# Kernel optimization log

Measured on AMD Instinct MI355X. Metric: run time of the kernel, lower is better.

The kernel has to match this reference:

```python
import jax, jax.numpy as jnp
import numpy as np

B, C, N = 4, 3, 8192

def setup_inputs() -> dict:
    key = jax.random.key(0)
    k1, k2, k3 = jax.random.split(key, 3)
    return {
        "registration_pred": jax.random.normal(k1, (B, C, N), dtype=jnp.float32),
        "registration_gt": jax.random.normal(k2, (B, C, N), dtype=jnp.float32),
        "coords": jax.random.normal(k3, (B, C, N), dtype=jnp.float32),
    }

def reference(registration_pred, registration_gt, coords):
    # point clouds: [B, N, 3]
    pc1 = jnp.transpose(coords + registration_gt, (0, 2, 1))   # gt cloud
    pc2 = jnp.transpose(coords + registration_pred, (0, 2, 1)) # generated cloud
    sq1 = jnp.sum(pc1 * pc1, axis=-1)  # [B, N]
    sq2 = jnp.sum(pc2 * pc2, axis=-1)  # [B, M]
    dist = (-2.0 * jnp.einsum('bnc,bmc->bnm', pc1, pc2)
            + sq1[:, :, None] + sq2[:, None, :])
    dist1 = jnp.min(dist, axis=-1)  # nearest gen point for each gt point [B, N]
    dist2 = jnp.min(dist, axis=1)   # nearest gt point for each gen point [B, M]
    return jnp.mean(jnp.sum(dist1, axis=1)) + jnp.mean(jnp.sum(dist2, axis=1))
```

## Files before the change

### kernel.cpp

```cpp
#include <hip/hip_runtime.h>
#include <cfloat>
#include <cstdint>

#define BB    4
#define NN    8192
#define NT    8
#define TPB   256
#define NTILE (NT*TPB)
#define NBQ   (NN/NTILE)
#define CPB   64
#define MS    (NN/CPB)

static __device__ __forceinline__ float vmin3(float a, float b, float c) {
    float r;
    asm("v_min3_f32 %0, %1, %2, %3" : "=v"(r) : "v"(a), "v"(b), "v"(c));
    return r;
}
static __device__ __forceinline__ float vmin2(float a, float b) {
    float r;
    asm("v_min_f32 %0, %1, %2" : "=v"(r) : "v"(a), "v"(b));
    return r;
}

__device__ __forceinline__ unsigned mapf(float f) {
    unsigned b = __float_as_uint(f);
    return b ^ ((unsigned)((int)b >> 31) | 0x80000000u);
}
__device__ __forceinline__ float unmapf(unsigned u) {
    unsigned b = u ^ (((u & 0x80000000u) != 0u) ? 0x80000000u : 0xFFFFFFFFu);
    return __uint_as_float(b);
}

__global__ __launch_bounds__(TPB, 6) void chamfer_onepass_kernel(
    const float* __restrict__ pred, const float* __restrict__ gt,
    const float* __restrict__ coords, unsigned* __restrict__ ws)
{
    const int b  = blockIdx.y;
    const int nb = blockIdx.x & (NBQ - 1);
    const int ms = blockIdx.x >> 2;
    const size_t base = (size_t)b * 3 * NN;
    const float* gr = gt     + base;
    const float* pr = pred   + base;
    const float* cc = coords + base;

    __shared__ float4 tile[CPB];

    const int tid = threadIdx.x;

    if (tid < CPB) {
        int m   = ms * CPB + tid;
        float x = cc[m]        + pr[m];
        float y = cc[NN + m]   + pr[NN + m];
        float z = cc[2*NN + m] + pr[2*NN + m];
        tile[tid] = make_float4(-2.f*x, -2.f*y, -2.f*z, fmaf(x, x, fmaf(y, y, z*z)));
    }

    float px[NT], py[NT], pz[NT], sqn[NT], mv[NT];
    const int n0 = nb * NTILE + tid;
    #pragma unroll
    for (int k = 0; k < NT; ++k) {
        int n   = n0 + k * TPB;
        float x = cc[n]        + gr[n];
        float y = cc[NN + n]   + gr[NN + n];
        float z = cc[2*NN + n] + gr[2*NN + n];
        px[k] = x; py[k] = y; pz[k] = z;
        sqn[k] = fmaf(x, x, fmaf(y, y, z*z));
        mv[k]  = FLT_MAX;
    }
    __syncthreads();

    const int lane = tid & 63;
    const int nxt  = (lane + 1) & 63;
    float cm = FLT_MAX;

    int jp = lane;
    float4 q = tile[jp];
    #pragma unroll 2
    for (int i = 0; i < CPB; ++i) {
        const int jn = (jp + 1) & (CPB - 1);
        float4 qn = tile[jn];
        float d[NT];
        #pragma unroll
        for (int k = 0; k < NT; ++k) {
            d[k]  = fmaf(px[k], q.x, fmaf(py[k], q.y, fmaf(pz[k], q.z, q.w + sqn[k])));
            mv[k] = vmin2(mv[k], d[k]);
        }
        float t = vmin3(d[0], d[1], d[2]);
        float u = vmin3(d[3], d[4], d[5]);
        float s = vmin3(d[6], d[7], t);
        float c = vmin2(s, u);
        cm = vmin2(__shfl(cm, nxt), c);
        jp = jn; q = qn;
    }

    unsigned* wsrow = ws + (size_t)b * NN;
    #pragma unroll
    for (int k = 0; k < NT; ++k)
        atomicMin(&wsrow[n0 + k * TPB], mapf(mv[k]));

    unsigned* wscol = ws + (size_t)BB * NN + (size_t)b * NN;
    const int cidx = (lane + CPB - 1) & (CPB - 1);
    atomicMin(&wscol[ms * CPB + cidx], mapf(cm));
}

__global__ __launch_bounds__(256) void ws_init_kernel(unsigned* __restrict__ ws)
{
    ((uint4*)ws)[blockIdx.x * 256 + threadIdx.x] = make_uint4(~0u, ~0u, ~0u, ~0u);
}

__global__ __launch_bounds__(256) void chamfer_reduce_a(
    const unsigned* __restrict__ ws, float* __restrict__ partial)
{
    int idx = blockIdx.x * 256 + threadIdx.x;
    const uint4* p = (const uint4*)ws;
    uint4 u = p[idx];
    float s = (unmapf(u.x) + unmapf(u.y)) + (unmapf(u.z) + unmapf(u.w));
    #pragma unroll
    for (int off = 32; off > 0; off >>= 1)
        s += __shfl_down(s, off);
    __shared__ float sm[4];
    if ((threadIdx.x & 63) == 0) sm[threadIdx.x >> 6] = s;
    __syncthreads();
    if (threadIdx.x == 0)
        partial[blockIdx.x] = (sm[0] + sm[1]) + (sm[2] + sm[3]);
}

__global__ __launch_bounds__(64) void chamfer_reduce_b(
    const float* __restrict__ partial, float* __restrict__ out)
{
    float s = partial[threadIdx.x];
    #pragma unroll
    for (int off = 32; off > 0; off >>= 1)
        s += __shfl_down(s, off);
    if (threadIdx.x == 0) out[0] = s * (1.0f / (float)BB);
}

extern "C" void kernel_launch(void* const* d_in, const int* in_sizes, int n_in,
                              void* d_out, int out_size, void* d_ws, size_t ws_size,
                              hipStream_t stream) {
    const float* pred   = (const float*)d_in[0];
    const float* gt     = (const float*)d_in[1];
    const float* coords = (const float*)d_in[2];
    unsigned*    wsu    = (unsigned*)d_ws;
    float*       part   = (float*)((char*)d_ws + (size_t)2 * BB * NN * sizeof(unsigned));
    float*       out    = (float*)d_out;

    ws_init_kernel<<<64, 256, 0, stream>>>(wsu);
    dim3 grid(NBQ * MS, BB);
    chamfer_onepass_kernel<<<grid, TPB, 0, stream>>>(pred, gt, coords, wsu);
    chamfer_reduce_a<<<64, 256, 0, stream>>>(wsu, part);
    chamfer_reduce_b<<<1, 64, 0, stream>>>(part, out);
}
```

Baseline: 45.28 us.

## Compute pairwise distances with split-bf16 MFMA and two directional passes

Replaces the scalar FMA distance loop with bf16 MFMA matrix ops. A prep kernel splits each coordinate, its -2x scaling and the squared norm into hi/lo bf16 parts, packed so a single 16x16x32 MFMA produces the full distance with compensated precision. Each direction (gt->pred and pred->gt) is computed as a separate row-min pass, which removes the atomics and the workspace init kernel. B tiles are double-buffered in LDS. In exchange the pairwise work is done twice, half the lanes feed zeros, and the split-bf16 scheme carries a rounding risk.

```diff
diff --git a/kernel.cpp b/kernel.cpp
--- a/kernel.cpp
+++ b/kernel.cpp
@@ -2,119 +2,150 @@
 #include <cfloat>
 #include <cstdint>
 
-#define BB    4
-#define NN    8192
-#define NT    8
-#define TPB   256
-#define NTILE (NT*TPB)
-#define NBQ   (NN/NTILE)
-#define CPB   64
-#define MS    (NN/CPB)
+#define BB 4
+#define NN 8192
 
-static __device__ __forceinline__ float vmin3(float a, float b, float c) {
-    float r;
-    asm("v_min3_f32 %0, %1, %2, %3" : "=v"(r) : "v"(a), "v"(b), "v"(c));
-    return r;
-}
+typedef short bf16x8 __attribute__((ext_vector_type(8)));
+typedef float f32x4  __attribute__((ext_vector_type(4)));
+
+#define ROW_OFF  0
+#define IMG_OFF  262144
+#define PART_OFF (262144 + 4*1048576)
+
 static __device__ __forceinline__ float vmin2(float a, float b) {
     float r;
     asm("v_min_f32 %0, %1, %2" : "=v"(r) : "v"(a), "v"(b));
     return r;
 }
-
-__device__ __forceinline__ unsigned mapf(float f) {
-    unsigned b = __float_as_uint(f);
-    return b ^ ((unsigned)((int)b >> 31) | 0x80000000u);
+__device__ __forceinline__ unsigned short btr(float v) {
+    return (unsigned short)(__float_as_uint(v) >> 16);
 }
-__device__ __forceinline__ float unmapf(unsigned u) {
-    unsigned b = u ^ (((u & 0x80000000u) != 0u) ? 0x80000000u : 0xFFFFFFFFu);
-    return __uint_as_float(b);
+__device__ __forceinline__ float bup(unsigned short h) {
+    return __uint_as_float(((unsigned)h) << 16);
+}
+__device__ __forceinline__ unsigned pk2(unsigned short a, unsigned short b) {
+    return (unsigned)a | ((unsigned)b << 16);
 }
 
-__global__ __launch_bounds__(TPB, 6) void chamfer_onepass_kernel(
+__global__ __launch_bounds__(256) void chamfer_prep_kernel(
     const float* __restrict__ pred, const float* __restrict__ gt,
-    const float* __restrict__ coords, unsigned* __restrict__ ws)
+    const float* __restrict__ coords, char* __restrict__ wsb)
 {
-    const int b  = blockIdx.y;
-    const int nb = blockIdx.x & (NBQ - 1);
-    const int ms = blockIdx.x >> 2;
-    const size_t base = (size_t)b * 3 * NN;
-    const float* gr = gt     + base;
-    const float* pr = pred   + base;
-    const float* cc = coords + base;
+    const int t = blockIdx.x * 256 + threadIdx.x;
+    const int cloud = t >> 15;
+    const int i = t & 32767;
+    const float* reg = cloud ? pred : gt;
+    const size_t base = (size_t)(i >> 13) * 3 * NN + (i & (NN - 1));
+    float x = coords[base]          + reg[base];
+    float y = coords[base + NN]     + reg[base + NN];
+    float z = coords[base + 2*NN]   + reg[base + 2*NN];
+    float sq = fmaf(x, x, fmaf(y, y, z * z));
+    unsigned short vhx = btr(x), vhy = btr(y), vhz = btr(z);
+    unsigned short vlx = btr(x - bup(vhx)), vly = btr(y - bup(vhy)), vlz = btr(z - bup(vhz));
+    unsigned short sh = btr(sq); float sr = sq - bup(sh);
+    unsigned short sm = btr(sr); unsigned short sl = btr(sr - bup(sm));
+    float ux = -2.f * x, uy = -2.f * y, uz = -2.f * z;
+    unsigned short uhx = btr(ux), uhy = btr(uy), uhz = btr(uz);
+    unsigned short ulx = btr(ux - bup(uhx)), uly = btr(uy - bup(uhy)), ulz = btr(uz - bup(uhz));
+    const unsigned short ONE = 0x3F80;
+    uint4 Ag0 = make_uint4(pk2(uhx, uhy), pk2(uhz, ulx), pk2(uly, ulz), pk2(sh, sm));
+    uint4 Ag1 = make_uint4(pk2(uhx, uhy), pk2(uhz, ONE), pk2(ONE, ONE), pk2(sl, 0));
+    uint4 Bg0 = make_uint4(pk2(vhx, vhy), pk2(vhz, vhx), pk2(vhy, vhz), pk2(ONE, ONE));
+    uint4 Bg1 = make_uint4(pk2(vlx, vly), pk2(vlz, sh), pk2(sm, sl), pk2(ONE, 0));
+    uint4* Aimg = (uint4*)(wsb + IMG_OFF + (size_t)cloud * 1048576);
+    uint4* Bimg = (uint4*)(wsb + IMG_OFF + 2097152 + (size_t)(1 - cloud) * 1048576);
+    Aimg[(size_t)i * 2]     = Ag0;  Aimg[(size_t)i * 2 + 1] = Ag1;
+    Bimg[(size_t)i * 2]     = Bg0;  Bimg[(size_t)i * 2 + 1] = Bg1;
+}
 
-    __shared__ float4 tile[CPB];
+__global__ __launch_bounds__(256) void chamfer_mfma_kernel(char* __restrict__ wsb)
+{
+    const int p = blockIdx.z, b = blockIdx.y, rg = blockIdx.x;
+    const int tid = threadIdx.x, w = tid >> 6, l = tid & 63;
+    const int lg = l >> 4, lr = l & 15;
+    const bool valid = lg < 2;
+    const uint4* Aimg = (const uint4*)(wsb + IMG_OFF + (size_t)p * 1048576);
+    const uint4* Bimg = (const uint4*)(wsb + IMG_OFF + 2097152 + (size_t)p * 1048576);
+    __shared__ uint4 sB[2][2048];
 
-    const int tid = threadIdx.x;
+    const int rbase = rg * 128 + w * 32;
+    bf16x8 a0 = {}, a1 = {};
+    if (valid) {
+        a0 = *(const bf16x8*)(Aimg + (size_t)(b * NN + rbase + lr) * 2 + lg);
+        a1 = *(const bf16x8*)(Aimg + (size_t)(b * NN + rbase + 16 + lr) * 2 + lg);
+    }
+    float r0[4], r1[4];
+    #pragma unroll
+    for (int j = 0; j < 4; ++j) { r0[j] = FLT_MAX; r1[j] = FLT_MAX; }
+    const f32x4 z4 = {0.f, 0.f, 0.f, 0.f};
 
-    if (tid < CPB) {
-        int m   = ms * CPB + tid;
-        float x = cc[m]        + pr[m];
-        float y = cc[NN + m]   + pr[NN + m];
-        float z = cc[2*NN + m] + pr[2*NN + m];
-        tile[tid] = make_float4(-2.f*x, -2.f*y, -2.f*z, fmaf(x, x, fmaf(y, y, z*z)));
+    const uint4* Bb = Bimg + (size_t)b * NN * 2;
+    uint4* s4 = &sB[0][0];
+    uint4 st[8];
+    #pragma unroll
+    for (int i = 0; i < 8; ++i) st[i] = Bb[i * 256 + tid];
+    #pragma unroll
+    for (int i = 0; i < 8; ++i) s4[i * 256 + tid] = st[i];
+    __syncthreads();
+
+    for (int c = 0; c < 8; ++c) {
+        if (c < 7) {
+            #pragma unroll
+            for (int i = 0; i < 8; ++i) st[i] = Bb[(c + 1) * 2048 + i * 256 + tid];
+        }
+        const uint4* cur = s4 + (c & 1) * 2048;
+        bf16x8 bf = {};
+        if (valid) bf = *(const bf16x8*)(cur + lr * 2 + lg);
+        #pragma unroll 4
+        for (int s = 0; s < 64; ++s) {
+            bf16x8 bn = {};
+            if (valid && s < 63)
+                bn = *(const bf16x8*)(cur + ((s + 1) * 16 + lr) * 2 + lg);
+            f32x4 d0 = __builtin_amdgcn_mfma_f32_16x16x32_bf16(a0, bf, z4, 0, 0, 0);
+            f32x4 d1 = __builtin_amdgcn_mfma_f32_16x16x32_bf16(a1, bf, z4, 0, 0, 0);
+            #pragma unroll
+            for (int j = 0; j < 4; ++j) {
+                r0[j] = vmin2(r0[j], d0[j]);
+                r1[j] = vmin2(r1[j], d1[j]);
+            }
+            bf = bn;
+        }
+        __syncthreads();
+        if (c < 7) {
+            #pragma unroll
+            for (int i = 0; i < 8; ++i) s4[((c + 1) & 1) * 2048 + i * 256 + tid] = st[i];
+        }
+        __syncthreads();
     }
 
-    float px[NT], py[NT], pz[NT], sqn[NT], mv[NT];
-    const int n0 = nb * NTILE + tid;
     #pragma unroll
-    for (int k = 0; k < NT; ++k) {
-        int n   = n0 + k * TPB;
-        float x = cc[n]        + gr[n];
-        float y = cc[NN + n]   + gr[NN + n];
-        float z = cc[2*NN + n] + gr[2*NN + n];
-        px[k] = x; py[k] = y; pz[k] = z;
-        sqn[k] = fmaf(x, x, fmaf(y, y, z*z));
-        mv[k]  = FLT_MAX;
+    for (int j = 0; j < 4; ++j) {
+        float v = r0[j];
+        v = vmin2(v, __shfl_xor(v, 1)); v = vmin2(v, __shfl_xor(v, 2));
+        v = vmin2(v, __shfl_xor(v, 4)); v = vmin2(v, __shfl_xor(v, 8));
+        r0[j] = v;
+        float u = r1[j];
+        u = vmin2(u, __shfl_xor(u, 1)); u = vmin2(u, __shfl_xor(u, 2));
+        u = vmin2(u, __shfl_xor(u, 4)); u = vmin2(u, __shfl_xor(u, 8));
+        r1[j] = u;
     }
-    __syncthreads();
-
-    const int lane = tid & 63;
-    const int nxt  = (lane + 1) & 63;
-    float cm = FLT_MAX;
-
-    int jp = lane;
-    float4 q = tile[jp];
-    #pragma unroll 2
-    for (int i = 0; i < CPB; ++i) {
-        const int jn = (jp + 1) & (CPB - 1);
-        float4 qn = tile[jn];
-        float d[NT];
+    if (lr == 0) {
+        float* rowpart = (float*)(wsb + ROW_OFF);
+        const size_t o = ((size_t)p * BB + b) * NN + rbase + lg * 4;
         #pragma unroll
-        for (int k = 0; k < NT; ++k) {
-            d[k]  = fmaf(px[k], q.x, fmaf(py[k], q.y, fmaf(pz[k], q.z, q.w + sqn[k])));
-            mv[k] = vmin2(mv[k], d[k]);
+        for (int j = 0; j < 4; ++j) {
+            rowpart[o + j]      = r0[j];
+            rowpart[o + 16 + j] = r1[j];
         }
-        float t = vmin3(d[0], d[1], d[2]);
-        float u = vmin3(d[3], d[4], d[5]);
-        float s = vmin3(d[6], d[7], t);
-        float c = vmin2(s, u);
-        cm = vmin2(__shfl(cm, nxt), c);
-        jp = jn; q = qn;
     }
-
-    unsigned* wsrow = ws + (size_t)b * NN;
-    #pragma unroll
-    for (int k = 0; k < NT; ++k)
-        atomicMin(&wsrow[n0 + k * TPB], mapf(mv[k]));
-
-    unsigned* wscol = ws + (size_t)BB * NN + (size_t)b * NN;
-    const int cidx = (lane + CPB - 1) & (CPB - 1);
-    atomicMin(&wscol[ms * CPB + cidx], mapf(cm));
-}
-
-__global__ __launch_bounds__(256) void ws_init_kernel(unsigned* __restrict__ ws)
-{
-    ((uint4*)ws)[blockIdx.x * 256 + threadIdx.x] = make_uint4(~0u, ~0u, ~0u, ~0u);
 }
 
 __global__ __launch_bounds__(256) void chamfer_reduce_a(
-    const unsigned* __restrict__ ws, float* __restrict__ partial)
+    const float* __restrict__ rp, float* __restrict__ partial)
 {
     int idx = blockIdx.x * 256 + threadIdx.x;
-    const uint4* p = (const uint4*)ws;
-    uint4 u = p[idx];
-    float s = (unmapf(u.x) + unmapf(u.y)) + (unmapf(u.z) + unmapf(u.w));
+    float4 u = ((const float4*)rp)[idx];
+    float s = (u.x + u.y) + (u.z + u.w);
     #pragma unroll
     for (int off = 32; off > 0; off >>= 1)
         s += __shfl_down(s, off);
@@ -141,13 +172,13 @@
     const float* pred   = (const float*)d_in[0];
     const float* gt     = (const float*)d_in[1];
     const float* coords = (const float*)d_in[2];
-    unsigned*    wsu    = (unsigned*)d_ws;
-    float*       part   = (float*)((char*)d_ws + (size_t)2 * BB * NN * sizeof(unsigned));
-    float*       out    = (float*)d_out;
+    char*  wsb  = (char*)d_ws;
+    float* part = (float*)(wsb + PART_OFF);
+    float* out  = (float*)d_out;
 
-    ws_init_kernel<<<64, 256, 0, stream>>>(wsu);
-    dim3 grid(NBQ * MS, BB);
-    chamfer_onepass_kernel<<<grid, TPB, 0, stream>>>(pred, gt, coords, wsu);
-    chamfer_reduce_a<<<64, 256, 0, stream>>>(wsu, part);
+    chamfer_prep_kernel<<<256, 256, 0, stream>>>(pred, gt, coords, wsb);
+    dim3 grid(64, BB, 2);
+    chamfer_mfma_kernel<<<grid, 256, 0, stream>>>(wsb);
+    chamfer_reduce_a<<<64, 256, 0, stream>>>((const float*)wsb, part);
     chamfer_reduce_b<<<1, 64, 0, stream>>>(part, out);
 }
```

After: 80.20 us. 77.1% more time.
